# Kernel optimization log

Hardware: AMD Instinct MI355X
Metric: run time of the kernel (lower is better)

The kernel has to match this reference:

```python
import jax, jax.numpy as jnp
import numpy as np

NUM_HEADS = 16


def setup_inputs() -> dict:
    key = jax.random.key(0)
    k1, k2, k3, k4 = jax.random.split(key, 4)
    B, N, C = 4, 1024, 1024
    x = jax.random.normal(k1, (B, N, C), dtype=jnp.float32)
    mask = jnp.ones((B, N), dtype=jnp.float32)  # 1 = visible token
    # 0.02 init scale keeps logits in a sane range (avoids saturated softmax)
    W_qkv = jax.random.normal(k2, (C, 3 * C), dtype=jnp.float32) * 0.02
    W_proj = jax.random.normal(k3, (C, C), dtype=jnp.float32) * 0.02
    b_proj = jax.random.normal(k4, (C,), dtype=jnp.float32) * 0.02
    return {"x": x, "mask": mask, "W_qkv": W_qkv, "W_proj": W_proj, "b_proj": b_proj}


def reference(x, mask, W_qkv, W_proj, b_proj):
    B, N, C = x.shape
    H = NUM_HEADS
    D = C // H
    scale = D ** -0.5
    qkv = (x @ W_qkv).reshape(B, N, 3, H, D)
    q, k, v = qkv[:, :, 0], qkv[:, :, 1], qkv[:, :, 2]  # each [B, N, H, D]
    attn = jnp.einsum("bnhd,bmhd->bhnm", q, k) * scale  # [B, H, N, N]
    attn = attn + (1.0 - mask)[:, None, None, :] * -5.0  # additive mask penalty
    attn = jax.nn.softmax(attn, axis=-1)
    out = jnp.einsum("bhnm,bmhd->bnhd", attn, v).reshape(B, N, C)
    return out @ W_proj + b_proj
```

## Files before the change

kernel.cpp:

```cpp
#include <hip/hip_runtime.h>

typedef __attribute__((ext_vector_type(8))) short bf16x8;
typedef __attribute__((ext_vector_type(4))) float f32x4;
typedef __attribute__((ext_vector_type(16))) float f32x16;
typedef __attribute__((ext_vector_type(4))) float fl4;
typedef __attribute__((ext_vector_type(8))) unsigned short u16x8;
typedef __attribute__((ext_vector_type(4))) unsigned short u16x4;
typedef __attribute__((ext_vector_type(2))) int i32x2;
typedef __attribute__((ext_vector_type(4))) int i32x4;

#define MFMA16(A,B,C) __builtin_amdgcn_mfma_f32_16x16x32_bf16((A),(B),(C),0,0,0)
#define MFMA32(A,B,C) __builtin_amdgcn_mfma_f32_32x32x16_bf16((A),(B),(C),0,0,0)

#if __has_builtin(__builtin_amdgcn_exp2f)
#define EXP2R(x) __builtin_amdgcn_exp2f(x)
#else
#define EXP2R(x) exp2f(x)
#endif

__device__ __forceinline__ unsigned short f2bf_bits(float x) {
  union { float f; unsigned u; } v; v.f = x;
  unsigned r = v.u + 0x7fffu + ((v.u >> 16) & 1u);
  return (unsigned short)(r >> 16);
}

__device__ __forceinline__ void gload_lds16(const void* g, void* l) {
  __builtin_amdgcn_global_load_lds((const __attribute__((address_space(1))) void*)g,
                                   (__attribute__((address_space(3))) void*)l, 16, 0, 0);
}

__device__ __forceinline__ bf16x8 lds_frag(const char* base, int row, int bir) {
  int off = (row << 7) + bir;
  off ^= (row & 7) << 4;
  return *(const bf16x8*)(base + off);
}

__device__ __forceinline__ int cvtpk_bf16(float a, float b) {
  int r; asm("v_cvt_pk_bf16_f32 %0, %1, %2" : "=v"(r) : "v"(a), "v"(b)); return r;
}

__device__ __forceinline__ void plswap(int& a, int& b) {
#if __has_builtin(__builtin_amdgcn_permlane32_swap)
  i32x2 r = __builtin_amdgcn_permlane32_swap(a, b, false, false);
  a = r[0]; b = r[1];
#else
  asm volatile("s_nop 1\n\tv_permlane32_swap_b32 %0, %1" : "+v"(a), "+v"(b));
#endif
}

__global__ __launch_bounds__(256) void k_prep(const float* __restrict__ x,
                                              unsigned short* __restrict__ xb,
                                              const float* __restrict__ wqkv,
                                              unsigned short* __restrict__ dqkv,
                                              const float* __restrict__ wproj,
                                              unsigned short* __restrict__ dproj) {
  __shared__ float tile[64][65];
  const int bid = blockIdx.x;
  const int t = threadIdx.x;
  if (bid < 2048) {
    int i = (bid * 256 + t) * 8;
    fl4 a = *(const fl4*)(x + i);
    fl4 b = *(const fl4*)(x + i + 4);
    u16x8 o;
    o[0] = f2bf_bits(a[0]); o[1] = f2bf_bits(a[1]); o[2] = f2bf_bits(a[2]); o[3] = f2bf_bits(a[3]);
    o[4] = f2bf_bits(b[0]); o[5] = f2bf_bits(b[1]); o[6] = f2bf_bits(b[2]); o[7] = f2bf_bits(b[3]);
    *(u16x8*)(xb + i) = o;
    return;
  }
  const int idx = bid - 2048;
  const int bx = idx & 63, by = idx >> 6;
  const float* src; unsigned short* dst; int NCOL, nt;
  if (bx < 48) { src = wqkv; dst = dqkv; NCOL = 3072; nt = bx * 64; }
  else         { src = wproj; dst = dproj; NCOL = 1024; nt = (bx - 48) * 64; }
  const float sc = (bx < 16) ? 0.18033688f : 1.0f;
  const int kt = by * 64;
  {
    int r = t >> 2, c0 = (t & 3) * 16;
    const float* s = src + (size_t)(kt + r) * NCOL + nt + c0;
    #pragma unroll
    for (int j = 0; j < 4; ++j) {
      fl4 v = *(const fl4*)(s + j * 4);
      tile[r][c0 + j * 4 + 0] = v[0]; tile[r][c0 + j * 4 + 1] = v[1];
      tile[r][c0 + j * 4 + 2] = v[2]; tile[r][c0 + j * 4 + 3] = v[3];
    }
  }
  __syncthreads();
  {
    int n = t >> 2, kc = (t & 3) * 16;
    unsigned short* d = dst + (size_t)(nt + n) * 1024 + kt + kc;
    u16x8 o0, o1;
    #pragma unroll
    for (int j = 0; j < 8; ++j) o0[j] = f2bf_bits(tile[kc + j][n] * sc);
    #pragma unroll
    for (int j = 0; j < 8; ++j) o1[j] = f2bf_bits(tile[kc + 8 + j][n] * sc);
    *(u16x8*)d = o0;
    *(u16x8*)(d + 8) = o1;
  }
}

template <int MODE>
__global__ __launch_bounds__(256) void k_gemm(const unsigned short* __restrict__ A,
                                              const unsigned short* __restrict__ Bt,
                                              unsigned short* __restrict__ qp,
                                              unsigned short* __restrict__ kp,
                                              unsigned short* __restrict__ vtp,
                                              const float* __restrict__ bias,
                                              float* __restrict__ outp) {
  __shared__ char lA[16384], lB[16384];
  const int tid = threadIdx.x, lane = tid & 63, w = tid >> 6;
  const int wm = w >> 1, wn = w & 1;
  const int m0 = blockIdx.y * 128, n0 = blockIdx.x * 128;
  const char* Ab = (const char*)A + (size_t)m0 * 2048;
  const char* Bb = (const char*)Bt + (size_t)n0 * 2048;

  f32x4 acc[4][4];
  #pragma unroll
  for (int mi = 0; mi < 4; ++mi)
    #pragma unroll
    for (int ni = 0; ni < 4; ++ni) acc[mi][ni] = f32x4{0.f, 0.f, 0.f, 0.f};

  for (int kt = 0; kt < 16; ++kt) {
    #pragma unroll
    for (int i = 0; i < 4; ++i) {
      int c = i * 256 + tid;
      int row = c >> 3, cc = c & 7, ccs = cc ^ (row & 7);
      char* dstA = lA + (i * 256 + w * 64) * 16;
      char* dstB = lB + (i * 256 + w * 64) * 16;
      gload_lds16(Ab + (size_t)row * 2048 + kt * 128 + ccs * 16, dstA);
      gload_lds16(Bb + (size_t)row * 2048 + kt * 128 + ccs * 16, dstB);
    }
    __syncthreads();
    #pragma unroll
    for (int ks = 0; ks < 2; ++ks) {
      bf16x8 af[4], bfv[4];
      #pragma unroll
      for (int mi = 0; mi < 4; ++mi)
        af[mi] = lds_frag(lA, wm * 64 + mi * 16 + (lane & 15), ks * 64 + ((lane >> 4) << 4));
      #pragma unroll
      for (int ni = 0; ni < 4; ++ni)
        bfv[ni] = lds_frag(lB, wn * 64 + ni * 16 + (lane & 15), ks * 64 + ((lane >> 4) << 4));
      #pragma unroll
      for (int mi = 0; mi < 4; ++mi)
        #pragma unroll
        for (int ni = 0; ni < 4; ++ni)
          acc[mi][ni] = MFMA16(af[mi], bfv[ni], acc[mi][ni]);
    }
    __syncthreads();
  }

  if (MODE == 0) {
    #pragma unroll
    for (int mi = 0; mi < 4; ++mi) {
      int row0 = m0 + wm * 64 + mi * 16 + ((lane >> 4) << 2);
      int bb = row0 >> 10, nn0 = row0 & 1023;
      #pragma unroll
      for (int ni = 0; ni < 4; ++ni) {
        int col = n0 + wn * 64 + ni * 16 + (lane & 15);
        int tt = col >> 10, rem = col & 1023, h = rem >> 6, d = rem & 63;
        f32x4 a = acc[mi][ni];
        if (tt == 2) {
          u16x4 pv;
          pv[0] = f2bf_bits(a[0]); pv[1] = f2bf_bits(a[1]);
          pv[2] = f2bf_bits(a[2]); pv[3] = f2bf_bits(a[3]);
          *(u16x4*)(vtp + (((size_t)(bb * 16 + h) * 64 + d) << 10) + nn0) = pv;
        } else {
          unsigned short* dst = (tt == 0) ? qp : kp;
          size_t base = ((size_t)(bb * 16 + h)) << 16;
          #pragma unroll
          for (int r = 0; r < 4; ++r)
            dst[base + (size_t)(nn0 + r) * 64 + d] = f2bf_bits(a[r]);
        }
      }
    }
  } else {
    #pragma unroll
    for (int mi = 0; mi < 4; ++mi) {
      int row0 = m0 + wm * 64 + mi * 16 + ((lane >> 4) << 2);
      #pragma unroll
      for (int ni = 0; ni < 4; ++ni) {
        int col = n0 + wn * 64 + ni * 16 + (lane & 15);
        float bv = bias[col];
        f32x4 a = acc[mi][ni];
        #pragma unroll
        for (int r = 0; r < 4; ++r)
          outp[(size_t)(row0 + r) * 1024 + col] = a[r] + bv;
      }
    }
  }
}

__global__ __launch_bounds__(512, 4) void k_attn(const unsigned short* __restrict__ qp,
                                                 const unsigned short* __restrict__ kp,
                                                 const unsigned short* __restrict__ vtp,
                                                 const float* __restrict__ mask,
                                                 unsigned short* __restrict__ aop) {
  __shared__ __align__(16) char lds[49152];
  const int tid = threadIdx.x, lane = tid & 63, w = tid >> 6;
  const int hi = lane >> 5, lq = lane & 31;
  const int pair = w >> 2, qsub = w & 3;
  const int g = blockIdx.x;
  const int bh = (g & 7) * 8 + ((g >> 6) & 7);
  const int qc = (g >> 3) & 7;
  const int b = bh >> 4, h = bh & 15;
  const char* kb = (const char*)(kp + ((size_t)bh << 16));
  const char* vb = (const char*)(vtp + ((size_t)bh << 16));
  const unsigned short* qh = qp + ((size_t)bh << 16);
  const float* mrow = mask + b * 1024 + pair * 512;
  const int q0 = qc * 128 + qsub * 32;

  const int kpk = tid >> 8, krow = (tid >> 3) & 31, kslot = tid & 7;
  const char* gK = kb + (size_t)kpk * 65536 + (size_t)krow * 128
                   + ((kslot ^ (krow & 7)) * 16);
  const int vpk = tid >> 8, vrow = (tid >> 2) & 63, vslot = tid & 3;
  const char* gV = vb + (size_t)vpk * 1024 + (size_t)vrow * 2048
                   + ((vslot ^ ((vrow >> 1) & 3)) * 16);
  char* const dK = lds + tid * 16;
  char* const dV = lds + 8192 + tid * 16;

  int kfo[4], vfo[4];
  #pragma unroll
  for (int dc = 0; dc < 4; ++dc)
    kfo[dc] = lq * 128 + (((dc << 1) | hi) ^ (lq & 7)) * 16;
  #pragma unroll
  for (int ks = 0; ks < 2; ++ks)
    #pragma unroll
    for (int nb = 0; nb < 2; ++nb) {
      int row = nb * 32 + lq;
      vfo[ks * 2 + nb] = row * 64 + (((ks << 1) | hi) ^ ((row >> 1) & 3)) * 16;
    }

  int bws[16];
  #pragma unroll
  for (int t2 = 0; t2 < 16; ++t2) {
    float mv = mrow[t2 * 32 + lq];
    bws[t2] = (hi == 0) ? (int)f2bf_bits(fmaf(mv, 7.2134752f, -12.9842554f)) : 0;
  }

  bf16x8 qB[4];
  #pragma unroll
  for (int dc = 0; dc < 4; ++dc)
    qB[dc] = *(const bf16x8*)(qh + (q0 + lq) * 64 + dc * 16 + hi * 8);

  i32x4 onesw = {hi == 0 ? 0x3F80 : 0, 0, 0, 0};
  const bf16x8 onesB = __builtin_bit_cast(bf16x8, onesw);

  f32x16 Z16;
  #pragma unroll
  for (int i = 0; i < 16; ++i) Z16[i] = 0.f;

  f32x16 O0, O1;
  #pragma unroll
  for (int i = 0; i < 16; ++i) { O0[i] = 0.f; O1[i] = 0.f; }
  float lsum = 0.f;

#define STAGE(BUF, T)                                                          \
  do {                                                                         \
    gload_lds16(gK + (T) * 4096, dK + (BUF) * 16384);                          \
    gload_lds16(gV + (T) * 64,   dV + (BUF) * 16384);                          \
  } while (0)

#define VMCNT(N) asm volatile("s_waitcnt vmcnt(" #N ")" ::: "memory")

#define STEP(BUF, T, N)                                                        \
  do {                                                                         \
    VMCNT(N);                                                                  \
    __builtin_amdgcn_s_barrier();                                              \
    if ((T) + 2 <= 15) STAGE(((T) + 2) % 3, (T) + 2);                          \
    const char* K = lds + (BUF) * 16384 + pair * 4096;                         \
    const char* V = lds + (BUF) * 16384 + 8192 + pair * 4096;                  \
    f32x16 acc;                                                                \
    {                                                                          \
      i32x4 bwv = {bws[T], 0, 0, 0};                                           \
      acc = MFMA32(__builtin_bit_cast(bf16x8, bwv), onesB, Z16);               \
    }                                                                          \
    __builtin_amdgcn_s_setprio(1);                                             \
    _Pragma("unroll") for (int dc = 0; dc < 4; ++dc) {                         \
      bf16x8 kf = *(const bf16x8*)(K + kfo[dc]);                               \
      acc = MFMA32(kf, qB[dc], acc);                                           \
    }                                                                          \
    __builtin_amdgcn_s_setprio(0);                                             \
    float p[16];                                                               \
    _Pragma("unroll") for (int r = 0; r < 16; ++r) {                           \
      p[r] = EXP2R(acc[r]);                                                    \
      lsum += p[r];                                                            \
    }                                                                          \
    int X0 = cvtpk_bf16(p[0], p[1]),   X1 = cvtpk_bf16(p[2], p[3]);            \
    int Y0 = cvtpk_bf16(p[4], p[5]),   Y1 = cvtpk_bf16(p[6], p[7]);            \
    int Z0 = cvtpk_bf16(p[8], p[9]),   Z1 = cvtpk_bf16(p[10], p[11]);          \
    int W0 = cvtpk_bf16(p[12], p[13]), W1 = cvtpk_bf16(p[14], p[15]);          \
    plswap(X0, Y0); plswap(X1, Y1);                                            \
    plswap(Z0, W0); plswap(Z1, W1);                                            \
    i32x4 pa0v = {X0, X1, Y0, Y1};                                             \
    i32x4 pa1v = {Z0, Z1, W0, W1};                                             \
    const bf16x8 PA0 = __builtin_bit_cast(bf16x8, pa0v);                       \
    const bf16x8 PA1 = __builtin_bit_cast(bf16x8, pa1v);                       \
    bf16x8 va0 = *(const bf16x8*)(V + vfo[0]);                                 \
    bf16x8 va1 = *(const bf16x8*)(V + vfo[1]);                                 \
    bf16x8 vb0 = *(const bf16x8*)(V + vfo[2]);                                 \
    bf16x8 vb1 = *(const bf16x8*)(V + vfo[3]);                                 \
    __builtin_amdgcn_s_setprio(1);                                             \
    O0 = MFMA32(PA0, va0, O0);                                                 \
    O1 = MFMA32(PA0, va1, O1);                                                 \
    O0 = MFMA32(PA1, vb0, O0);                                                 \
    O1 = MFMA32(PA1, vb1, O1);                                                 \
    __builtin_amdgcn_s_setprio(0);                                             \
  } while (0)

  STAGE(0, 0);
  STAGE(1, 1);
  STEP(0, 0, 2);  STEP(1, 1, 2);  STEP(2, 2, 2);  STEP(0, 3, 2);
  STEP(1, 4, 2);  STEP(2, 5, 2);  STEP(0, 6, 2);  STEP(1, 7, 2);
  STEP(2, 8, 2);  STEP(0, 9, 2);  STEP(1, 10, 2); STEP(2, 11, 2);
  STEP(0, 12, 2); STEP(1, 13, 2); STEP(2, 14, 2); STEP(0, 15, 0);
#undef STEP
#undef VMCNT
#undef STAGE

  __syncthreads();
  float tot = lsum + __shfl_xor(lsum, 32);
  float* fx = (float*)lds;
  if (pair == 1) {
    int base = qsub * 64 * 34 + lane * 34;
    #pragma unroll
    for (int r = 0; r < 16; ++r) { fx[base + r] = O0[r]; fx[base + 16 + r] = O1[r]; }
    fx[base + 32] = tot;
  }
  __syncthreads();
  if (pair == 0) {
    int base = qsub * 64 * 34 + lane * 34;
    float invT = 1.0f / (tot + fx[base + 32]);
    #pragma unroll
    for (int r = 0; r < 16; ++r) {
      int qr = (r & 3) + 8 * (r >> 2) + 4 * hi;
      float iv = __shfl(invT, qr);
      float o0 = (O0[r] + fx[base + r]) * iv;
      float o1 = (O1[r] + fx[base + 16 + r]) * iv;
      size_t ob = (size_t)(b * 1024 + q0 + qr) * 1024 + h * 64 + lq;
      aop[ob] = f2bf_bits(o0);
      aop[ob + 32] = f2bf_bits(o1);
    }
  }
}

extern "C" void kernel_launch(void* const* d_in, const int* in_sizes, int n_in,
                              void* d_out, int out_size, void* d_ws, size_t ws_size,
                              hipStream_t stream) {
  const float* x     = (const float*)d_in[0];
  const float* mask  = (const float*)d_in[1];
  const float* wqkv  = (const float*)d_in[2];
  const float* wproj = (const float*)d_in[3];
  const float* bproj = (const float*)d_in[4];
  float* out = (float*)d_out;

  char* ws = (char*)d_ws;
  unsigned short* xb     = (unsigned short*)(ws);
  unsigned short* wqkvt  = (unsigned short*)(ws + 8388608);
  unsigned short* wprojt = (unsigned short*)(ws + 14680064);
  unsigned short* qbuf   = (unsigned short*)(ws + 16777216);
  unsigned short* kbuf   = (unsigned short*)(ws + 25165824);
  unsigned short* vtbuf  = (unsigned short*)(ws + 33554432);
  unsigned short* aobuf  = (unsigned short*)(ws + 41943040);

  k_prep<<<dim3(3072), dim3(256), 0, stream>>>(x, xb, wqkv, wqkvt, wproj, wprojt);
  k_gemm<0><<<dim3(24, 32), dim3(256), 0, stream>>>(xb, wqkvt, qbuf, kbuf, vtbuf, nullptr, nullptr);
  k_attn<<<dim3(512), dim3(512), 0, stream>>>(qbuf, kbuf, vtbuf, mask, aobuf);
  k_gemm<1><<<dim3(8, 32), dim3(256), 0, stream>>>(aobuf, wprojt, nullptr, nullptr, nullptr, bproj, out);
}
```

Before: 95.35 us.

## Triple-buffer GEMM LDS tiles with async global-to-LDS prefetch pipeline

Replaces the single-buffered GEMM main loop, which had two barriers per K-tile, with a three-stage ring buffer of 32-wide K slices. Global-to-LDS loads for later stages are issued while earlier stages are computed, synchronised with vmcnt waits and one barrier per step. The LDS layout changes to a row-pair packing with an XOR swizzle on 4 chunks, and fragment offsets are precomputed. This uses more LDS (48KB), which may reduce occupancy, and adds manual waitcnt logic that must count outstanding loads exactly.

```diff
diff --git a/kernel.cpp b/kernel.cpp
--- a/kernel.cpp
+++ b/kernel.cpp
@@ -27,12 +27,6 @@
 __device__ __forceinline__ void gload_lds16(const void* g, void* l) {
   __builtin_amdgcn_global_load_lds((const __attribute__((address_space(1))) void*)g,
                                    (__attribute__((address_space(3))) void*)l, 16, 0, 0);
-}
-
-__device__ __forceinline__ bf16x8 lds_frag(const char* base, int row, int bir) {
-  int off = (row << 7) + bir;
-  off ^= (row & 7) << 4;
-  return *(const bf16x8*)(base + off);
 }
 
 __device__ __forceinline__ int cvtpk_bf16(float a, float b) {
@@ -106,47 +100,81 @@
                                               unsigned short* __restrict__ vtp,
                                               const float* __restrict__ bias,
                                               float* __restrict__ outp) {
-  __shared__ char lA[16384], lB[16384];
+  __shared__ __align__(16) char lds[49152];
   const int tid = threadIdx.x, lane = tid & 63, w = tid >> 6;
   const int wm = w >> 1, wn = w & 1;
   const int m0 = blockIdx.y * 128, n0 = blockIdx.x * 128;
   const char* Ab = (const char*)A + (size_t)m0 * 2048;
   const char* Bb = (const char*)Bt + (size_t)n0 * 2048;
 
+  int goff[2];
+  #pragma unroll
+  for (int i = 0; i < 2; ++i) {
+    int c = i * 256 + tid;
+    int lr = c >> 3, s = c & 7, p = s >> 2, kc = (s & 3) ^ (lr & 3);
+    goff[i] = (((lr << 1) | p) * 2048) + (kc << 4);
+  }
+
+  int afo[4], bfo[4];
+  #pragma unroll
+  for (int mi = 0; mi < 4; ++mi) {
+    int tr = wm * 64 + mi * 16 + (lane & 15), kc = lane >> 4;
+    afo[mi] = (tr >> 1) * 128 + (tr & 1) * 64 + (((kc ^ ((tr >> 1) & 3))) << 4);
+  }
+  #pragma unroll
+  for (int ni = 0; ni < 4; ++ni) {
+    int tr = wn * 64 + ni * 16 + (lane & 15), kc = lane >> 4;
+    bfo[ni] = (tr >> 1) * 128 + (tr & 1) * 64 + (((kc ^ ((tr >> 1) & 3))) << 4);
+  }
+
   f32x4 acc[4][4];
   #pragma unroll
   for (int mi = 0; mi < 4; ++mi)
     #pragma unroll
     for (int ni = 0; ni < 4; ++ni) acc[mi][ni] = f32x4{0.f, 0.f, 0.f, 0.f};
 
-  for (int kt = 0; kt < 16; ++kt) {
-    #pragma unroll
-    for (int i = 0; i < 4; ++i) {
-      int c = i * 256 + tid;
-      int row = c >> 3, cc = c & 7, ccs = cc ^ (row & 7);
-      char* dstA = lA + (i * 256 + w * 64) * 16;
-      char* dstB = lB + (i * 256 + w * 64) * 16;
-      gload_lds16(Ab + (size_t)row * 2048 + kt * 128 + ccs * 16, dstA);
-      gload_lds16(Bb + (size_t)row * 2048 + kt * 128 + ccs * 16, dstB);
-    }
-    __syncthreads();
-    #pragma unroll
-    for (int ks = 0; ks < 2; ++ks) {
-      bf16x8 af[4], bfv[4];
-      #pragma unroll
-      for (int mi = 0; mi < 4; ++mi)
-        af[mi] = lds_frag(lA, wm * 64 + mi * 16 + (lane & 15), ks * 64 + ((lane >> 4) << 4));
-      #pragma unroll
-      for (int ni = 0; ni < 4; ++ni)
-        bfv[ni] = lds_frag(lB, wn * 64 + ni * 16 + (lane & 15), ks * 64 + ((lane >> 4) << 4));
-      #pragma unroll
-      for (int mi = 0; mi < 4; ++mi)
-        #pragma unroll
-        for (int ni = 0; ni < 4; ++ni)
-          acc[mi][ni] = MFMA16(af[mi], bfv[ni], acc[mi][ni]);
-    }
-    __syncthreads();
-  }
+#define GSTAGE(BUF, T)                                                         \
+  do {                                                                         \
+    char* dA = lds + (BUF) * 16384 + tid * 16;                                 \
+    char* dB = dA + 8192;                                                      \
+    gload_lds16(Ab + goff[0] + (T) * 64, dA);                                  \
+    gload_lds16(Ab + goff[1] + (T) * 64, dA + 4096);                           \
+    gload_lds16(Bb + goff[0] + (T) * 64, dB);                                  \
+    gload_lds16(Bb + goff[1] + (T) * 64, dB + 4096);                           \
+  } while (0)
+
+#define GCOMP(BUF)                                                             \
+  do {                                                                         \
+    const char* LA = lds + (BUF) * 16384;                                      \
+    const char* LB = LA + 8192;                                                \
+    bf16x8 af[4], bfv[4];                                                      \
+    _Pragma("unroll") for (int mi = 0; mi < 4; ++mi)                           \
+      af[mi] = *(const bf16x8*)(LA + afo[mi]);                                 \
+    _Pragma("unroll") for (int ni = 0; ni < 4; ++ni)                           \
+      bfv[ni] = *(const bf16x8*)(LB + bfo[ni]);                                \
+    _Pragma("unroll") for (int mi = 0; mi < 4; ++mi)                           \
+      _Pragma("unroll") for (int ni = 0; ni < 4; ++ni)                         \
+        acc[mi][ni] = MFMA16(af[mi], bfv[ni], acc[mi][ni]);                    \
+  } while (0)
+
+  GSTAGE(0, 0);
+  GSTAGE(1, 1);
+  {
+    int bc = 0, bs = 2;
+    for (int j = 0; j < 31; ++j) {
+      asm volatile("s_waitcnt vmcnt(4)" ::: "memory");
+      __builtin_amdgcn_s_barrier();
+      if (j < 30) GSTAGE(bs, j + 2);
+      GCOMP(bc);
+      bc = (bc == 2) ? 0 : bc + 1;
+      bs = (bs == 2) ? 0 : bs + 1;
+    }
+    asm volatile("s_waitcnt vmcnt(0)" ::: "memory");
+    __builtin_amdgcn_s_barrier();
+    GCOMP(1);
+  }
+#undef GCOMP
+#undef GSTAGE
 
   if (MODE == 0) {
     #pragma unroll
```

Result: faster. 91.37 us (-4.2%).
